# Kernel optimization log

Measured on AMD Instinct MI355X. Metric: run time of the kernel, lower is better.

## Reference

```python
import jax, jax.numpy as jnp
import numpy as np

B, T, D, H = 256, 512, 128, 256

def setup_inputs() -> dict:
    key = jax.random.key(0)
    ks = jax.random.split(key, 6)
    s = lambda n: 1.0 / np.sqrt(n)
    return {
        "x":  jax.random.normal(ks[0], (B, T, D), jnp.float32),
        "Wx": jax.random.normal(ks[1], (D, 4 * H), jnp.float32) * s(D),
        "Wh": jax.random.normal(ks[2], (H, 4 * H), jnp.float32) * s(H),
        "b":  jnp.zeros((4 * H,), jnp.float32),
        "W1": jax.random.normal(ks[3], (H, H), jnp.float32) * s(H),
        "b1": jnp.zeros((H,), jnp.float32),
        "W2": jax.random.normal(ks[4], (H, H), jnp.float32) * s(H),
        "b2": jnp.zeros((H,), jnp.float32),
        "W3": jax.random.normal(ks[5], (H, 1), jnp.float32) * s(H),
        "b3": jnp.zeros((1,), jnp.float32),
    }

def reference(x, Wx, Wh, b, W1, b1, W2, b2, W3, b3):
    # Precompute input projections for all timesteps: [B, T, 4H]
    xproj = jnp.einsum('btd,dg->btg', x, Wx) + b

    def step(carry, xp_t):
        h, c = carry
        gates = xp_t + h @ Wh  # [B, 4H]
        i, f, g, o = jnp.split(gates, 4, axis=-1)  # Keras order: i, f, c, o
        i = jax.nn.sigmoid(i)
        f = jax.nn.sigmoid(f)
        o = jax.nn.sigmoid(o)
        c_new = f * c + i * jnp.tanh(g)
        h_new = o * jnp.tanh(c_new)
        # per-step MLP head
        y = jnp.tanh(h_new @ W1 + b1)
        y = jnp.tanh(y @ W2 + b2)
        y = y @ W3 + b3  # [B, 1]
        return (h_new, c_new), y

    h0 = jnp.zeros((x.shape[0], Wh.shape[0]), x.dtype)
    c0 = jnp.zeros_like(h0)
    _, ys = jax.lax.scan(step, (h0, c0), jnp.swapaxes(xproj, 0, 1))  # ys: [T, B, 1]
    return jnp.swapaxes(ys, 0, 1)  # [B, T, 1]
```

## Files before the change

### kernel.cpp

```cpp
#include <hip/hip_runtime.h>

typedef _Float16 half8 __attribute__((ext_vector_type(8)));
typedef float f32x4 __attribute__((ext_vector_type(4)));

union H8U { unsigned long long u[2]; half8 v; };

__device__ __forceinline__ float fast_sigmoid(float v) {
  return 1.0f / (1.0f + __expf(-v));
}
__device__ __forceinline__ float fast_tanh(float v) {
  return 2.0f / (1.0f + __expf(-2.0f * v)) - 1.0f;
}

#define AL(p) __hip_atomic_load((p), __ATOMIC_RELAXED, __HIP_MEMORY_SCOPE_AGENT)

__global__ void __launch_bounds__(256) prep_kernel(
    const float* __restrict__ W1, const float* __restrict__ W2,
    _Float16* __restrict__ W1f, _Float16* __restrict__ W2f,
    unsigned* __restrict__ flags)
{
  int idx = blockIdx.x * 256 + threadIdx.x;
  if (idx < 256)
    __hip_atomic_store(&flags[idx], 0u, __ATOMIC_RELAXED, __HIP_MEMORY_SCOPE_AGENT);
  int m  = idx >> 16;
  int i2 = idx & 65535;
  int s = i2 & 7, lane = (i2 >> 3) & 63, ks = (i2 >> 9) & 7, ct = (i2 >> 12) & 15;
  int col = ct * 16 + (lane & 15);
  int k   = ks * 32 + (lane >> 4) * 8 + s;
  float v = (m == 0) ? W1[k * 256 + col] : W2[k * 256 + col];
  _Float16* dst = (m == 0) ? W1f : W2f;
  dst[i2] = (_Float16)v;
}

__global__ void __launch_bounds__(256, 1) lstm_rec_kernel(
    const float* __restrict__ x, const float* __restrict__ Wx,
    const float* __restrict__ Wh, const float* __restrict__ bias,
    _Float16* __restrict__ h_all, unsigned* __restrict__ flags)
{
  __shared__ __align__(16) _Float16 Wt[8 * 12 * 64 * 8];
  __shared__ __align__(16) _Float16 At[2 * 12 * 64 * 8];
  __shared__ float pre_s[32][132];
  __shared__ float c_s[32][33];
  __shared__ __align__(16) _Float16 h_s[32][32];
  __shared__ float bias_s[128];

  const int tid = threadIdx.x;
  const int g  = blockIdx.x & 7;
  const int j  = blockIdx.x >> 3;
  const int b0 = g * 32;

  for (int idx = tid; idx < 384 * 128; idx += 256) {
    int k = idx >> 7, c = idx & 127;
    int q = c >> 5, d = c & 31;
    int gc = q * 256 + j * 32 + d;
    float v = (k < 128) ? Wx[k * 1024 + gc] : Wh[(k - 128) * 1024 + gc];
    int ct = c >> 4, lcol = c & 15;
    int ks = k >> 5, kg = (k >> 3) & 3, s = k & 7;
    Wt[(((ct * 12 + ks) * 64) + kg * 16 + lcol) * 8 + s] = (_Float16)v;
  }
  if (tid < 128) {
    int q = tid >> 5, d = tid & 31;
    bias_s[tid] = bias[q * 256 + j * 32 + d];
  }
  for (int i = tid; i < 32 * 33; i += 256) ((float*)c_s)[i] = 0.f;

  const int lane = tid & 63, wid = tid >> 6;
  const int rt = wid & 1;
  const int c4 = (wid >> 1) * 4;
  const int prow = rt * 16 + ((lane >> 4) << 2);
  const int pc = lane & 15;

  const int srow = tid >> 3, sseg = tid & 7;
  const int s_rt = srow >> 4, s_lrow = srow & 15;

  const half8* Ap = (const half8*)At + rt * 768 + lane;

  const float4* xb = (const float4*)x + (size_t)(b0 + srow) * 16384 + sseg * 4;
  float4 XR[4];
  XR[0] = xb[0]; XR[1] = xb[1]; XR[2] = xb[2]; XR[3] = xb[3];

  __syncthreads();

  half8 Bv[48];
  {
    const half8* Bb = (const half8*)Wt + c4 * 768 + lane;
    #pragma unroll
    for (int i = 0; i < 48; ++i) Bv[i] = Bb[(i >> 3) * 768 + (i & 7)];
  }
  {
    const half8* Bb = (const half8*)Wt + c4 * 768 + lane;
    #pragma unroll
    for (int ct = 0; ct < 4; ++ct)
      #pragma unroll
      for (int ks = 0; ks < 12; ++ks)
        Bv[ct * 12 + ks] = Bb[ct * 768 + ks * 64];
  }

  f32x4 accx0, accx1, accx2, accx3;

  {
    half8 p0, p1;
    p0[0] = (_Float16)XR[0].x; p0[1] = (_Float16)XR[0].y;
    p0[2] = (_Float16)XR[0].z; p0[3] = (_Float16)XR[0].w;
    p0[4] = (_Float16)XR[1].x; p0[5] = (_Float16)XR[1].y;
    p0[6] = (_Float16)XR[1].z; p0[7] = (_Float16)XR[1].w;
    p1[0] = (_Float16)XR[2].x; p1[1] = (_Float16)XR[2].y;
    p1[2] = (_Float16)XR[2].z; p1[3] = (_Float16)XR[2].w;
    p1[4] = (_Float16)XR[3].x; p1[5] = (_Float16)XR[3].y;
    p1[6] = (_Float16)XR[3].z; p1[7] = (_Float16)XR[3].w;
    int xi = (s_rt * 12 + (sseg >> 1)) * 64 + ((sseg & 1) * 2) * 16 + s_lrow;
    ((half8*)At)[xi] = p0; ((half8*)At)[xi + 16] = p1;
  }
  __syncthreads();
  {
    accx0 = (f32x4){0.f, 0.f, 0.f, 0.f}; accx1 = accx0; accx2 = accx0; accx3 = accx0;
    #pragma unroll
    for (int ks = 0; ks < 4; ++ks) {
      half8 av = Ap[ks * 64];
      accx0 = __builtin_amdgcn_mfma_f32_16x16x32_f16(av, Bv[0 * 12 + ks], accx0, 0, 0, 0);
      accx1 = __builtin_amdgcn_mfma_f32_16x16x32_f16(av, Bv[1 * 12 + ks], accx1, 0, 0, 0);
      accx2 = __builtin_amdgcn_mfma_f32_16x16x32_f16(av, Bv[2 * 12 + ks], accx2, 0, 0, 0);
      accx3 = __builtin_amdgcn_mfma_f32_16x16x32_f16(av, Bv[3 * 12 + ks], accx3, 0, 0, 0);
    }
  }
  XR[0] = xb[32]; XR[1] = xb[33]; XR[2] = xb[34]; XR[3] = xb[35];

  for (int t = 0; t < 512; ++t) {
    if (t > 0) {
      int iters = 0;
      while (true) {
        unsigned v = (lane < 8) ? AL(&flags[g * 16 + lane]) : (unsigned)t;
        if (__ballot(v >= (unsigned)t) == ~0ull) break;
        if (++iters > (1 << 17)) break;
        __builtin_amdgcn_s_sleep(1);
      }
      const unsigned long long* hp = (const unsigned long long*)h_all +
          ((size_t)(t - 1) * 256 + b0 + srow) * 64 + sseg * 8;
      H8U c0, c1, c2, c3;
      c0.u[0] = AL(hp + 0); c0.u[1] = AL(hp + 1);
      c1.u[0] = AL(hp + 2); c1.u[1] = AL(hp + 3);
      c2.u[0] = AL(hp + 4); c2.u[1] = AL(hp + 5);
      c3.u[0] = AL(hp + 6); c3.u[1] = AL(hp + 7);
      int hb = (s_rt * 12 + 4 + sseg) * 64 + s_lrow;
      ((half8*)At)[hb +  0] = c0.v; ((half8*)At)[hb + 16] = c1.v;
      ((half8*)At)[hb + 32] = c2.v; ((half8*)At)[hb + 48] = c3.v;
    } else {
      H8U zz; zz.u[0] = 0ull; zz.u[1] = 0ull;
      int hb = (s_rt * 12 + 4 + sseg) * 64 + s_lrow;
      ((half8*)At)[hb +  0] = zz.v; ((half8*)At)[hb + 16] = zz.v;
      ((half8*)At)[hb + 32] = zz.v; ((half8*)At)[hb + 48] = zz.v;
    }
    __syncthreads();

    {
      f32x4 a0 = accx0, a1 = accx1, a2 = accx2, a3 = accx3;
      #pragma unroll
      for (int ks = 4; ks < 12; ++ks) {
        half8 av = Ap[ks * 64];
        a0 = __builtin_amdgcn_mfma_f32_16x16x32_f16(av, Bv[0 * 12 + ks], a0, 0, 0, 0);
        a1 = __builtin_amdgcn_mfma_f32_16x16x32_f16(av, Bv[1 * 12 + ks], a1, 0, 0, 0);
        a2 = __builtin_amdgcn_mfma_f32_16x16x32_f16(av, Bv[2 * 12 + ks], a2, 0, 0, 0);
        a3 = __builtin_amdgcn_mfma_f32_16x16x32_f16(av, Bv[3 * 12 + ks], a3, 0, 0, 0);
      }
      #pragma unroll
      for (int r = 0; r < 4; ++r) {
        pre_s[prow + r][(c4 + 0) * 16 + pc] = a0[r];
        pre_s[prow + r][(c4 + 1) * 16 + pc] = a1[r];
        pre_s[prow + r][(c4 + 2) * 16 + pc] = a2[r];
        pre_s[prow + r][(c4 + 3) * 16 + pc] = a3[r];
      }
    }
    __syncthreads();

    #pragma unroll
    for (int ii = 0; ii < 4; ++ii) {
      int d = sseg + 8 * ii;
      float iv = fast_sigmoid(pre_s[srow][d]      + bias_s[d]);
      float fv = fast_sigmoid(pre_s[srow][32 + d] + bias_s[32 + d]);
      float gv = fast_tanh   (pre_s[srow][64 + d] + bias_s[64 + d]);
      float ov = fast_sigmoid(pre_s[srow][96 + d] + bias_s[96 + d]);
      float cv = fv * c_s[srow][d] + iv * gv;
      c_s[srow][d] = cv;
      h_s[srow][d] = (_Float16)(ov * fast_tanh(cv));
    }
    __syncthreads();

    {
      unsigned long long hv = ((const unsigned long long*)h_s)[tid];
      unsigned long long* hp = (unsigned long long*)h_all +
          ((size_t)t * 256 + b0 + (tid >> 3)) * 64 + j * 8 + (tid & 7);
      __hip_atomic_store(hp, hv, __ATOMIC_RELAXED, __HIP_MEMORY_SCOPE_AGENT);
    }
    __syncthreads();

    if (tid == 0)
      __hip_atomic_store(&flags[g * 16 + j], (unsigned)(t + 1),
                         __ATOMIC_RELEASE, __HIP_MEMORY_SCOPE_AGENT);

    if (t < 511) {
      {
        half8 p0, p1;
        p0[0] = (_Float16)XR[0].x; p0[1] = (_Float16)XR[0].y;
        p0[2] = (_Float16)XR[0].z; p0[3] = (_Float16)XR[0].w;
        p0[4] = (_Float16)XR[1].x; p0[5] = (_Float16)XR[1].y;
        p0[6] = (_Float16)XR[1].z; p0[7] = (_Float16)XR[1].w;
        p1[0] = (_Float16)XR[2].x; p1[1] = (_Float16)XR[2].y;
        p1[2] = (_Float16)XR[2].z; p1[3] = (_Float16)XR[2].w;
        p1[4] = (_Float16)XR[3].x; p1[5] = (_Float16)XR[3].y;
        p1[6] = (_Float16)XR[3].z; p1[7] = (_Float16)XR[3].w;
        int xi = (s_rt * 12 + (sseg >> 1)) * 64 + ((sseg & 1) * 2) * 16 + s_lrow;
        ((half8*)At)[xi] = p0; ((half8*)At)[xi + 16] = p1;
      }
      __syncthreads();
      {
        accx0 = (f32x4){0.f, 0.f, 0.f, 0.f}; accx1 = accx0; accx2 = accx0; accx3 = accx0;
        #pragma unroll
        for (int ks = 0; ks < 4; ++ks) {
          half8 av = Ap[ks * 64];
          accx0 = __builtin_amdgcn_mfma_f32_16x16x32_f16(av, Bv[0 * 12 + ks], accx0, 0, 0, 0);
          accx1 = __builtin_amdgcn_mfma_f32_16x16x32_f16(av, Bv[1 * 12 + ks], accx1, 0, 0, 0);
          accx2 = __builtin_amdgcn_mfma_f32_16x16x32_f16(av, Bv[2 * 12 + ks], accx2, 0, 0, 0);
          accx3 = __builtin_amdgcn_mfma_f32_16x16x32_f16(av, Bv[3 * 12 + ks], accx3, 0, 0, 0);
        }
      }
      int tn = (t + 2 < 512) ? (t + 2) : 511;
      XR[0] = xb[(size_t)tn * 32 + 0]; XR[1] = xb[(size_t)tn * 32 + 1];
      XR[2] = xb[(size_t)tn * 32 + 2]; XR[3] = xb[(size_t)tn * 32 + 3];
    }
  }
}

__device__ __forceinline__ void head_gemm(const _Float16* __restrict__ A,
                                          const _Float16* __restrict__ Wf,
                                          const float* __restrict__ bvec,
                                          _Float16* __restrict__ Yd,
                                          int lane, int w)
{
  const half8* Af = (const half8*)A + w * 512 + lane;
  for (int ct = 0; ct < 16; ++ct) {
    const half8* Bf = (const half8*)Wf + ct * 512 + lane;
    f32x4 acc = {0.f, 0.f, 0.f, 0.f};
    #pragma unroll
    for (int ks = 0; ks < 8; ++ks)
      acc = __builtin_amdgcn_mfma_f32_16x16x32_f16(Af[ks * 64], Bf[ks * 64], acc, 0, 0, 0);
    int col = ct * 16 + (lane & 15);
    float bb = bvec[col];
    int ks2 = col >> 5, kg2 = (col >> 3) & 3, s2 = col & 7;
    #pragma unroll
    for (int r = 0; r < 4; ++r) {
      int row = w * 16 + ((lane >> 4) << 2) + r;
      float v = fast_tanh(acc[r] + bb);
      Yd[(((w * 8 + ks2) * 64) + kg2 * 16 + (row & 15)) * 8 + s2] = (_Float16)v;
    }
  }
}

__global__ void __launch_bounds__(256) head_kernel(
    const _Float16* __restrict__ h_all,
    const _Float16* __restrict__ W1f, const _Float16* __restrict__ W2f,
    const float* __restrict__ b1, const float* __restrict__ b2,
    const float* __restrict__ W3, const float* __restrict__ b3,
    float* __restrict__ out)
{
  __shared__ __align__(16) _Float16 A_s[16384];
  __shared__ __align__(16) _Float16 Y_s[16384];
  const int tid = threadIdx.x;
  const size_t r0 = (size_t)blockIdx.x * 64;

  {
    int row = tid >> 2, seg = tid & 3;
    int rtl = row >> 4, lrow = row & 15;
    const half8* hp = (const half8*)(h_all + (r0 + row) * 256 + seg * 64);
    #pragma unroll
    for (int i = 0; i < 8; ++i) {
      int k0 = seg * 64 + i * 8;
      int ks = k0 >> 5, kg = (k0 >> 3) & 3;
      ((half8*)A_s)[(rtl * 8 + ks) * 64 + kg * 16 + lrow] = hp[i];
    }
  }
  __syncthreads();

  const int lane = tid & 63, w = tid >> 6;
  head_gemm(A_s, W1f, b1, Y_s, lane, w);
  __syncthreads();
  head_gemm(Y_s, W2f, b2, A_s, lane, w);
  __syncthreads();

  {
    int row = tid >> 2, part = tid & 3;
    int rtl = row >> 4, lrow = row & 15;
    float p = 0.f;
    #pragma unroll
    for (int kk = 0; kk < 8; ++kk) {
      int k0 = part * 64 + kk * 8;
      int ks = k0 >> 5, kg = (k0 >> 3) & 3;
      half8 y = ((const half8*)A_s)[(rtl * 8 + ks) * 64 + kg * 16 + lrow];
      #pragma unroll
      for (int i = 0; i < 8; ++i) p += (float)y[i] * W3[k0 + i];
    }
    p += __shfl_xor(p, 1);
    p += __shfl_xor(p, 2);
    if (part == 0) {
      size_t r = r0 + row;
      int tt = (int)(r >> 8), bb = (int)(r & 255);
      out[(size_t)bb * 512 + tt] = p + b3[0];
    }
  }
}

extern "C" void kernel_launch(void* const* d_in, const int* in_sizes, int n_in,
                              void* d_out, int out_size, void* d_ws, size_t ws_size,
                              hipStream_t stream)
{
  const float* x  = (const float*)d_in[0];
  const float* Wx = (const float*)d_in[1];
  const float* Wh = (const float*)d_in[2];
  const float* b  = (const float*)d_in[3];
  const float* W1 = (const float*)d_in[4];
  const float* b1 = (const float*)d_in[5];
  const float* W2 = (const float*)d_in[6];
  const float* b2 = (const float*)d_in[7];
  const float* W3 = (const float*)d_in[8];
  const float* b3 = (const float*)d_in[9];
  float* out = (float*)d_out;

  char* ws = (char*)d_ws;
  unsigned* flags  = (unsigned*)ws;
  _Float16* W1f    = (_Float16*)(ws + 4096);
  _Float16* W2f    = (_Float16*)(ws + 4096 + 131072);
  _Float16* h_all  = (_Float16*)(ws + 4096 + 262144);
  if (ws_size < (size_t)4096 + 262144 + 67108864) return;

  hipLaunchKernelGGL(prep_kernel, dim3(512), dim3(256), 0, stream,
                     W1, W2, W1f, W2f, flags);
  hipLaunchKernelGGL(lstm_rec_kernel, dim3(64), dim3(256), 0, stream,
                     x, Wx, Wh, b, h_all, flags);
  hipLaunchKernelGGL(head_kernel, dim3(2048), dim3(256), 0, stream,
                     h_all, W1f, W2f, b1, b2, W3, b3, out);
}
```

Baseline: 1.960 ms.

## Replace flag barrier with sequence-tagged h exchange and in-register gate math

Drops the per-block flag counters. Each hidden value is now written into a double-buffered exchange array together with its timestep tag in the upper 16 bits, and consumers spin directly on the data words until every tag matches. This removes a release store, a separate flag poll and a dependent data load from the critical path of each step. Gate activations and the cell state also move from shared memory into registers by remapping the wave/column assignment, which eliminates two block barriers per step. A XOR swizzle is applied to the shared A tile to reduce bank conflicts. In exchange, polling without sleep adds memory traffic, and a memset of the exchange buffer is needed before each launch.

```diff
diff --git a/kernel.cpp b/kernel.cpp
--- a/kernel.cpp
+++ b/kernel.cpp
@@ -3,7 +3,7 @@
 typedef _Float16 half8 __attribute__((ext_vector_type(8)));
 typedef float f32x4 __attribute__((ext_vector_type(4)));
 
-union H8U { unsigned long long u[2]; half8 v; };
+union H8U { unsigned long long u[2]; half8 v; unsigned short s[8]; };
 
 __device__ __forceinline__ float fast_sigmoid(float v) {
   return 1.0f / (1.0f + __expf(-v));
@@ -12,16 +12,15 @@
   return 2.0f / (1.0f + __expf(-2.0f * v)) - 1.0f;
 }
 
-#define AL(p) __hip_atomic_load((p), __ATOMIC_RELAXED, __HIP_MEMORY_SCOPE_AGENT)
+#define AL(p)    __hip_atomic_load((p), __ATOMIC_RELAXED, __HIP_MEMORY_SCOPE_AGENT)
+#define AS(p, x) __hip_atomic_store((p), (x), __ATOMIC_RELAXED, __HIP_MEMORY_SCOPE_AGENT)
+#define SWZ(i) ((i) ^ (((i) >> 6) & 7))
 
 __global__ void __launch_bounds__(256) prep_kernel(
     const float* __restrict__ W1, const float* __restrict__ W2,
-    _Float16* __restrict__ W1f, _Float16* __restrict__ W2f,
-    unsigned* __restrict__ flags)
+    _Float16* __restrict__ W1f, _Float16* __restrict__ W2f)
 {
   int idx = blockIdx.x * 256 + threadIdx.x;
-  if (idx < 256)
-    __hip_atomic_store(&flags[idx], 0u, __ATOMIC_RELAXED, __HIP_MEMORY_SCOPE_AGENT);
   int m  = idx >> 16;
   int i2 = idx & 65535;
   int s = i2 & 7, lane = (i2 >> 3) & 63, ks = (i2 >> 9) & 7, ct = (i2 >> 12) & 15;
@@ -35,14 +34,10 @@
 __global__ void __launch_bounds__(256, 1) lstm_rec_kernel(
     const float* __restrict__ x, const float* __restrict__ Wx,
     const float* __restrict__ Wh, const float* __restrict__ bias,
-    _Float16* __restrict__ h_all, unsigned* __restrict__ flags)
+    unsigned* __restrict__ hx, _Float16* __restrict__ h_all)
 {
   __shared__ __align__(16) _Float16 Wt[8 * 12 * 64 * 8];
   __shared__ __align__(16) _Float16 At[2 * 12 * 64 * 8];
-  __shared__ float pre_s[32][132];
-  __shared__ float c_s[32][33];
-  __shared__ __align__(16) _Float16 h_s[32][32];
-  __shared__ float bias_s[128];
 
   const int tid = threadIdx.x;
   const int g  = blockIdx.x & 7;
@@ -58,22 +53,18 @@
     int ks = k >> 5, kg = (k >> 3) & 3, s = k & 7;
     Wt[(((ct * 12 + ks) * 64) + kg * 16 + lcol) * 8 + s] = (_Float16)v;
   }
-  if (tid < 128) {
-    int q = tid >> 5, d = tid & 31;
-    bias_s[tid] = bias[q * 256 + j * 32 + d];
-  }
-  for (int i = tid; i < 32 * 33; i += 256) ((float*)c_s)[i] = 0.f;
 
   const int lane = tid & 63, wid = tid >> 6;
-  const int rt = wid & 1;
-  const int c4 = (wid >> 1) * 4;
+  const int rt = wid & 1, e = wid >> 1;
   const int prow = rt * 16 + ((lane >> 4) << 2);
   const int pc = lane & 15;
+  const int gdim = j * 32 + e * 16 + pc;
+
+  const float bv0 = bias[0 * 256 + gdim], bv1 = bias[1 * 256 + gdim],
+              bv2 = bias[2 * 256 + gdim], bv3 = bias[3 * 256 + gdim];
 
   const int srow = tid >> 3, sseg = tid & 7;
   const int s_rt = srow >> 4, s_lrow = srow & 15;
-
-  const half8* Ap = (const half8*)At + rt * 768 + lane;
 
   const float4* xb = (const float4*)x + (size_t)(b0 + srow) * 16384 + sseg * 4;
   float4 XR[4];
@@ -83,20 +74,17 @@
 
   half8 Bv[48];
   {
-    const half8* Bb = (const half8*)Wt + c4 * 768 + lane;
-    #pragma unroll
-    for (int i = 0; i < 48; ++i) Bv[i] = Bb[(i >> 3) * 768 + (i & 7)];
-  }
-  {
-    const half8* Bb = (const half8*)Wt + c4 * 768 + lane;
-    #pragma unroll
-    for (int ct = 0; ct < 4; ++ct)
+    const half8* Wp = (const half8*)Wt;
+    #pragma unroll
+    for (int q = 0; q < 4; ++q)
       #pragma unroll
       for (int ks = 0; ks < 12; ++ks)
-        Bv[ct * 12 + ks] = Bb[ct * 768 + ks * 64];
-  }
-
-  f32x4 accx0, accx1, accx2, accx3;
+        Bv[q * 12 + ks] = Wp[(2 * q + e) * 768 + ks * 64 + lane];
+  }
+
+  half8* Ag = (half8*)At;
+  float cst[4] = {0.f, 0.f, 0.f, 0.f};
+  f32x4 ax0, ax1, ax2, ax3;
 
   {
     half8 p0, p1;
@@ -109,119 +97,116 @@
     p1[4] = (_Float16)XR[3].x; p1[5] = (_Float16)XR[3].y;
     p1[6] = (_Float16)XR[3].z; p1[7] = (_Float16)XR[3].w;
     int xi = (s_rt * 12 + (sseg >> 1)) * 64 + ((sseg & 1) * 2) * 16 + s_lrow;
-    ((half8*)At)[xi] = p0; ((half8*)At)[xi + 16] = p1;
-  }
-  __syncthreads();
-  {
-    accx0 = (f32x4){0.f, 0.f, 0.f, 0.f}; accx1 = accx0; accx2 = accx0; accx3 = accx0;
+    Ag[SWZ(xi)] = p0; Ag[SWZ(xi + 16)] = p1;
+  }
+  __syncthreads();
+  {
+    ax0 = (f32x4){0.f, 0.f, 0.f, 0.f}; ax1 = ax0; ax2 = ax0; ax3 = ax0;
     #pragma unroll
     for (int ks = 0; ks < 4; ++ks) {
-      half8 av = Ap[ks * 64];
-      accx0 = __builtin_amdgcn_mfma_f32_16x16x32_f16(av, Bv[0 * 12 + ks], accx0, 0, 0, 0);
-      accx1 = __builtin_amdgcn_mfma_f32_16x16x32_f16(av, Bv[1 * 12 + ks], accx1, 0, 0, 0);
-      accx2 = __builtin_amdgcn_mfma_f32_16x16x32_f16(av, Bv[2 * 12 + ks], accx2, 0, 0, 0);
-      accx3 = __builtin_amdgcn_mfma_f32_16x16x32_f16(av, Bv[3 * 12 + ks], accx3, 0, 0, 0);
+      half8 av = Ag[SWZ(rt * 768 + ks * 64 + lane)];
+      ax0 = __builtin_amdgcn_mfma_f32_16x16x32_f16(av, Bv[0 * 12 + ks], ax0, 0, 0, 0);
+      ax1 = __builtin_amdgcn_mfma_f32_16x16x32_f16(av, Bv[1 * 12 + ks], ax1, 0, 0, 0);
+      ax2 = __builtin_amdgcn_mfma_f32_16x16x32_f16(av, Bv[2 * 12 + ks], ax2, 0, 0, 0);
+      ax3 = __builtin_amdgcn_mfma_f32_16x16x32_f16(av, Bv[3 * 12 + ks], ax3, 0, 0, 0);
     }
   }
   XR[0] = xb[32]; XR[1] = xb[33]; XR[2] = xb[34]; XR[3] = xb[35];
 
   for (int t = 0; t < 512; ++t) {
+    const int hbase = (s_rt * 12 + 4 + sseg) * 64 + s_lrow;
     if (t > 0) {
+      const unsigned long long* hp = (const unsigned long long*)hx +
+          (((t - 1) & 1) ? 32768 : 0) + (size_t)(b0 + srow) * 128 + sseg * 16;
+      unsigned long long vv[16];
+      const unsigned long long msk  = 0xFFFF0000FFFF0000ull;
+      const unsigned long long want = ((unsigned long long)(unsigned)t << 16) |
+                                      ((unsigned long long)(unsigned)t << 48);
       int iters = 0;
       while (true) {
-        unsigned v = (lane < 8) ? AL(&flags[g * 16 + lane]) : (unsigned)t;
-        if (__ballot(v >= (unsigned)t) == ~0ull) break;
+        #pragma unroll
+        for (int i = 0; i < 16; ++i) vv[i] = AL(hp + i);
+        unsigned long long diff = 0;
+        #pragma unroll
+        for (int i = 0; i < 16; ++i) diff |= (vv[i] & msk) ^ want;
+        if (diff == 0) break;
         if (++iters > (1 << 17)) break;
-        __builtin_amdgcn_s_sleep(1);
       }
-      const unsigned long long* hp = (const unsigned long long*)h_all +
-          ((size_t)(t - 1) * 256 + b0 + srow) * 64 + sseg * 8;
-      H8U c0, c1, c2, c3;
-      c0.u[0] = AL(hp + 0); c0.u[1] = AL(hp + 1);
-      c1.u[0] = AL(hp + 2); c1.u[1] = AL(hp + 3);
-      c2.u[0] = AL(hp + 4); c2.u[1] = AL(hp + 5);
-      c3.u[0] = AL(hp + 6); c3.u[1] = AL(hp + 7);
-      int hb = (s_rt * 12 + 4 + sseg) * 64 + s_lrow;
-      ((half8*)At)[hb +  0] = c0.v; ((half8*)At)[hb + 16] = c1.v;
-      ((half8*)At)[hb + 32] = c2.v; ((half8*)At)[hb + 48] = c3.v;
+      H8U pk[4];
+      #pragma unroll
+      for (int i = 0; i < 16; ++i) {
+        pk[i >> 2].s[(2 * i) & 7]     = (unsigned short)vv[i];
+        pk[i >> 2].s[(2 * i + 1) & 7] = (unsigned short)(vv[i] >> 32);
+      }
+      #pragma unroll
+      for (int kg = 0; kg < 4; ++kg) Ag[SWZ(hbase + kg * 16)] = pk[kg].v;
     } else {
       H8U zz; zz.u[0] = 0ull; zz.u[1] = 0ull;
-      int hb = (s_rt * 12 + 4 + sseg) * 64 + s_lrow;
-      ((half8*)At)[hb +  0] = zz.v; ((half8*)At)[hb + 16] = zz.v;
-      ((half8*)At)[hb + 32] = zz.v; ((half8*)At)[hb + 48] = zz.v;
+      #pragma unroll
+      for (int kg = 0; kg < 4; ++kg) Ag[SWZ(hbase + kg * 16)] = zz.v;
     }
     __syncthreads();
 
+    f32x4 a0 = ax0, a1 = ax1, a2 = ax2, a3 = ax3;
+    #pragma unroll
+    for (int ks = 4; ks < 12; ++ks) {
+      half8 av = Ag[SWZ(rt * 768 + ks * 64 + lane)];
+      a0 = __builtin_amdgcn_mfma_f32_16x16x32_f16(av, Bv[0 * 12 + ks], a0, 0, 0, 0);
+      a1 = __builtin_amdgcn_mfma_f32_16x16x32_f16(av, Bv[1 * 12 + ks], a1, 0, 0, 0);
+      a2 = __builtin_amdgcn_mfma_f32_16x16x32_f16(av, Bv[2 * 12 + ks], a2, 0, 0, 0);
+      a3 = __builtin_amdgcn_mfma_f32_16x16x32_f16(av, Bv[3 * 12 + ks], a3, 0, 0, 0);
+    }
+
+    unsigned hw[4]; unsigned short hfb[4];
+    #pragma unroll
+    for (int r = 0; r < 4; ++r) {
+      float iv = fast_sigmoid(a0[r] + bv0);
+      float fv = fast_sigmoid(a1[r] + bv1);
+      float gv = fast_tanh   (a2[r] + bv2);
+      float ov = fast_sigmoid(a3[r] + bv3);
+      cst[r] = fv * cst[r] + iv * gv;
+      float hv = ov * fast_tanh(cst[r]);
+      _Float16 hf = (_Float16)hv;
+      unsigned short hb_; __builtin_memcpy(&hb_, &hf, 2);
+      hfb[r] = hb_;
+      hw[r] = ((unsigned)(t + 1) << 16) | (unsigned)hb_;
+    }
+
+    if (t < 511) {
+      half8 p0, p1;
+      p0[0] = (_Float16)XR[0].x; p0[1] = (_Float16)XR[0].y;
+      p0[2] = (_Float16)XR[0].z; p0[3] = (_Float16)XR[0].w;
+      p0[4] = (_Float16)XR[1].x; p0[5] = (_Float16)XR[1].y;
+      p0[6] = (_Float16)XR[1].z; p0[7] = (_Float16)XR[1].w;
+      p1[0] = (_Float16)XR[2].x; p1[1] = (_Float16)XR[2].y;
+      p1[2] = (_Float16)XR[2].z; p1[3] = (_Float16)XR[2].w;
+      p1[4] = (_Float16)XR[3].x; p1[5] = (_Float16)XR[3].y;
+      p1[6] = (_Float16)XR[3].z; p1[7] = (_Float16)XR[3].w;
+      int xi = (s_rt * 12 + (sseg >> 1)) * 64 + ((sseg & 1) * 2) * 16 + s_lrow;
+      Ag[SWZ(xi)] = p0; Ag[SWZ(xi + 16)] = p1;
+    }
+    __syncthreads();
+
     {
-      f32x4 a0 = accx0, a1 = accx1, a2 = accx2, a3 = accx3;
-      #pragma unroll
-      for (int ks = 4; ks < 12; ++ks) {
-        half8 av = Ap[ks * 64];
-        a0 = __builtin_amdgcn_mfma_f32_16x16x32_f16(av, Bv[0 * 12 + ks], a0, 0, 0, 0);
-        a1 = __builtin_amdgcn_mfma_f32_16x16x32_f16(av, Bv[1 * 12 + ks], a1, 0, 0, 0);
-        a2 = __builtin_amdgcn_mfma_f32_16x16x32_f16(av, Bv[2 * 12 + ks], a2, 0, 0, 0);
-        a3 = __builtin_amdgcn_mfma_f32_16x16x32_f16(av, Bv[3 * 12 + ks], a3, 0, 0, 0);
+      unsigned* hxp = hx + ((t & 1) ? 65536 : 0) + (size_t)(b0 + prow) * 256 + gdim;
+      _Float16* hap = h_all + ((size_t)t * 256 + b0 + prow) * 256 + gdim;
+      #pragma unroll
+      for (int r = 0; r < 4; ++r) {
+        AS(hxp + (size_t)r * 256, hw[r]);
+        _Float16 hval; __builtin_memcpy(&hval, &hfb[r], 2);
+        hap[(size_t)r * 256] = hval;
       }
-      #pragma unroll
-      for (int r = 0; r < 4; ++r) {
-        pre_s[prow + r][(c4 + 0) * 16 + pc] = a0[r];
-        pre_s[prow + r][(c4 + 1) * 16 + pc] = a1[r];
-        pre_s[prow + r][(c4 + 2) * 16 + pc] = a2[r];
-        pre_s[prow + r][(c4 + 3) * 16 + pc] = a3[r];
-      }
-    }
-    __syncthreads();
-
-    #pragma unroll
-    for (int ii = 0; ii < 4; ++ii) {
-      int d = sseg + 8 * ii;
-      float iv = fast_sigmoid(pre_s[srow][d]      + bias_s[d]);
-      float fv = fast_sigmoid(pre_s[srow][32 + d] + bias_s[32 + d]);
-      float gv = fast_tanh   (pre_s[srow][64 + d] + bias_s[64 + d]);
-      float ov = fast_sigmoid(pre_s[srow][96 + d] + bias_s[96 + d]);
-      float cv = fv * c_s[srow][d] + iv * gv;
-      c_s[srow][d] = cv;
-      h_s[srow][d] = (_Float16)(ov * fast_tanh(cv));
-    }
-    __syncthreads();
-
-    {
-      unsigned long long hv = ((const unsigned long long*)h_s)[tid];
-      unsigned long long* hp = (unsigned long long*)h_all +
-          ((size_t)t * 256 + b0 + (tid >> 3)) * 64 + j * 8 + (tid & 7);
-      __hip_atomic_store(hp, hv, __ATOMIC_RELAXED, __HIP_MEMORY_SCOPE_AGENT);
-    }
-    __syncthreads();
-
-    if (tid == 0)
-      __hip_atomic_store(&flags[g * 16 + j], (unsigned)(t + 1),
-                         __ATOMIC_RELEASE, __HIP_MEMORY_SCOPE_AGENT);
+    }
 
     if (t < 511) {
-      {
-        half8 p0, p1;
-        p0[0] = (_Float16)XR[0].x; p0[1] = (_Float16)XR[0].y;
-        p0[2] = (_Float16)XR[0].z; p0[3] = (_Float16)XR[0].w;
-        p0[4] = (_Float16)XR[1].x; p0[5] = (_Float16)XR[1].y;
-        p0[6] = (_Float16)XR[1].z; p0[7] = (_Float16)XR[1].w;
-        p1[0] = (_Float16)XR[2].x; p1[1] = (_Float16)XR[2].y;
-        p1[2] = (_Float16)XR[2].z; p1[3] = (_Float16)XR[2].w;
-        p1[4] = (_Float16)XR[3].x; p1[5] = (_Float16)XR[3].y;
-        p1[6] = (_Float16)XR[3].z; p1[7] = (_Float16)XR[3].w;
-        int xi = (s_rt * 12 + (sseg >> 1)) * 64 + ((sseg & 1) * 2) * 16 + s_lrow;
-        ((half8*)At)[xi] = p0; ((half8*)At)[xi + 16] = p1;
-      }
-      __syncthreads();
-      {
-        accx0 = (f32x4){0.f, 0.f, 0.f, 0.f}; accx1 = accx0; accx2 = accx0; accx3 = accx0;
-        #pragma unroll
-        for (int ks = 0; ks < 4; ++ks) {
-          half8 av = Ap[ks * 64];
-          accx0 = __builtin_amdgcn_mfma_f32_16x16x32_f16(av, Bv[0 * 12 + ks], accx0, 0, 0, 0);
-          accx1 = __builtin_amdgcn_mfma_f32_16x16x32_f16(av, Bv[1 * 12 + ks], accx1, 0, 0, 0);
-          accx2 = __builtin_amdgcn_mfma_f32_16x16x32_f16(av, Bv[2 * 12 + ks], accx2, 0, 0, 0);
-          accx3 = __builtin_amdgcn_mfma_f32_16x16x32_f16(av, Bv[3 * 12 + ks], accx3, 0, 0, 0);
-        }
+      ax0 = (f32x4){0.f, 0.f, 0.f, 0.f}; ax1 = ax0; ax2 = ax0; ax3 = ax0;
+      #pragma unroll
+      for (int ks = 0; ks < 4; ++ks) {
+        half8 av = Ag[SWZ(rt * 768 + ks * 64 + lane)];
+        ax0 = __builtin_amdgcn_mfma_f32_16x16x32_f16(av, Bv[0 * 12 + ks], ax0, 0, 0, 0);
+        ax1 = __builtin_amdgcn_mfma_f32_16x16x32_f16(av, Bv[1 * 12 + ks], ax1, 0, 0, 0);
+        ax2 = __builtin_amdgcn_mfma_f32_16x16x32_f16(av, Bv[2 * 12 + ks], ax2, 0, 0, 0);
+        ax3 = __builtin_amdgcn_mfma_f32_16x16x32_f16(av, Bv[3 * 12 + ks], ax3, 0, 0, 0);
       }
       int tn = (t + 2 < 512) ? (t + 2) : 511;
       XR[0] = xb[(size_t)tn * 32 + 0]; XR[1] = xb[(size_t)tn * 32 + 1];
@@ -325,16 +310,17 @@
   float* out = (float*)d_out;
 
   char* ws = (char*)d_ws;
-  unsigned* flags  = (unsigned*)ws;
-  _Float16* W1f    = (_Float16*)(ws + 4096);
-  _Float16* W2f    = (_Float16*)(ws + 4096 + 131072);
-  _Float16* h_all  = (_Float16*)(ws + 4096 + 262144);
-  if (ws_size < (size_t)4096 + 262144 + 67108864) return;
-
+  unsigned*  hx    = (unsigned*)ws;
+  _Float16*  W1f   = (_Float16*)(ws + 524288);
+  _Float16*  W2f   = (_Float16*)(ws + 655360);
+  _Float16*  h_all = (_Float16*)(ws + 786432);
+  if (ws_size < (size_t)786432 + 67108864) return;
+
+  hipMemsetAsync(hx, 0, 524288, stream);
   hipLaunchKernelGGL(prep_kernel, dim3(512), dim3(256), 0, stream,
-                     W1, W2, W1f, W2f, flags);
+                     W1, W2, W1f, W2f);
   hipLaunchKernelGGL(lstm_rec_kernel, dim3(64), dim3(256), 0, stream,
-                     x, Wx, Wh, b, h_all, flags);
+                     x, Wx, Wh, b, hx, h_all);
   hipLaunchKernelGGL(head_kernel, dim3(2048), dim3(256), 0, stream,
                      h_all, W1f, W2f, b1, b2, W3, b3, out);
 }
```

After: 2.172 ms. 1.11x slower.
